# Optimization experiments

Hardware: AMD Instinct MI355X
Metric: run time of the kernel (lower is better)

Reference implementation:

```python
import jax, jax.numpy as jnp
import numpy as np

B, T_ENC, D_IN = 64, 32, 4096
T_DEC, D_WORD = 20, 300
H = 512
VOCAB = 20000


def lstm_scan(x_tbd, W, b, c0, h0):
    """TF BasicLSTMCell (forget_bias=1.0, gate order i,j,f,o) scanned over time.
    x_tbd: [T,B,D]; W: [D+H, 4H]; returns (c,h) final state and all h [T,B,H]."""
    def step(carry, x):
        c, h = carry
        z = jnp.concatenate([x, h], axis=-1) @ W + b  # [B,4H]
        i, j, f, o = jnp.split(z, 4, axis=-1)
        c = c * jax.nn.sigmoid(f + 1.0) + jax.nn.sigmoid(i) * jnp.tanh(j)
        h = jnp.tanh(c) * jax.nn.sigmoid(o)
        return (c, h), h
    (c, h), hs = jax.lax.scan(step, (c0, h0), x_tbd)
    return (c, h), hs


def setup_inputs() -> dict:
    key = jax.random.key(0)
    ks = jax.random.split(key, 8)
    frames = jax.random.normal(ks[0], (B, T_ENC, D_IN), dtype=jnp.float32)
    caption = jax.random.randint(ks[1], (B, T_DEC), 0, VOCAB, dtype=jnp.int32)
    embeddings = jax.random.normal(ks[2], (VOCAB, D_WORD), dtype=jnp.float32) * 0.1
    s_enc = 1.0 / np.sqrt(D_IN + H)
    s_dec = 1.0 / np.sqrt(D_WORD + H)
    W_enc = jax.random.normal(ks[3], (D_IN + H, 4 * H), dtype=jnp.float32) * s_enc
    b_enc = jnp.zeros((4 * H,), dtype=jnp.float32)
    W_dec = jax.random.normal(ks[4], (D_WORD + H, 4 * H), dtype=jnp.float32) * s_dec
    b_dec = jnp.zeros((4 * H,), dtype=jnp.float32)
    W_proj = jax.random.normal(ks[5], (H, D_WORD), dtype=jnp.float32) / np.sqrt(H)
    b_proj = jnp.zeros((D_WORD,), dtype=jnp.float32)
    return {"frames": frames, "embeddings": embeddings, "W_enc": W_enc,
            "b_enc": b_enc, "W_dec": W_dec, "b_dec": b_dec,
            "W_proj": W_proj, "b_proj": b_proj, "caption": caption}


def reference(frames, embeddings, W_enc, b_enc, W_dec, b_dec, W_proj, b_proj, caption):
    b = frames.shape[0]
    c0 = jnp.zeros((b, H), dtype=frames.dtype)
    h0 = jnp.zeros((b, H), dtype=frames.dtype)
    # encoder over frames (dropout keep_prob=1 -> identity)
    (c, h), _ = lstm_scan(jnp.swapaxes(frames, 0, 1), W_enc, b_enc, c0, h0)
    # teacher-forced decoder over caption embeddings
    cap_emb = embeddings[caption]                      # [B,T_dec,D_word]
    _, hs = lstm_scan(jnp.swapaxes(cap_emb, 0, 1), W_dec, b_dec, c, h)  # [T,B,H]
    # per-step shared dense hidden->word, vectorized over time
    word_vecs = hs @ W_proj + b_proj                   # [T,B,D_word]
    return jnp.swapaxes(word_vecs, 0, 1)               # [B,T_dec,D_word]
```

## Files before the change

kernel.cpp:

```cpp
#include <hip/hip_runtime.h>
#include <hip/hip_bf16.h>

#define BATCH  64
#define T_ENC  32
#define D_IN   4096
#define T_DEC  20
#define D_WORD 300
#define HID    512
#define FOURH  2048
#define NWG    64
#define FPAD   32
#define ZP     13
#define CNT_BASE 2048
#define FLAGS_N  3520

typedef __attribute__((ext_vector_type(8))) short short8;
typedef __attribute__((ext_vector_type(4))) float f32x4;
typedef unsigned long long ull;

static __device__ __forceinline__ unsigned short f2bf(float f){
  union { float f; unsigned u; } v; v.f = f;
  unsigned r = v.u + 0x7fffu + ((v.u >> 16) & 1u);
  return (unsigned short)(r >> 16);
}
static __device__ __forceinline__ float bf2f(unsigned short b){
  union { unsigned u; float f; } v; v.u = ((unsigned)b) << 16;
  return v.f;
}
static __device__ __forceinline__ float sigm(float x){
  return __builtin_amdgcn_rcpf(1.f + __expf(-x));
}
static __device__ __forceinline__ float tanh_f(float x){
  float e = __expf(2.f * x);
  return 1.f - 2.f * __builtin_amdgcn_rcpf(e + 1.f);
}

__global__ __launch_bounds__(256) void prep(
    const float* __restrict__ frames, const float* __restrict__ W_enc,
    unsigned short* __restrict__ fb, unsigned short* __restrict__ wt,
    unsigned* __restrict__ flags, float* __restrict__ Xe)
{
  const int g = blockIdx.x * 256 + threadIdx.x;
  if (blockIdx.x == 0){
    for (int i = threadIdx.x; i < FLAGS_N; i += 256)
      __hip_atomic_store(&flags[i], 0u, __ATOMIC_RELAXED, __HIP_MEMORY_SCOPE_AGENT);
  }
  {
    float2 z2; z2.x = 0.f; z2.y = 0.f;
    *(float2*)(Xe + (long)g * 2) = z2;
  }
  if (g < 1048576){
    const long base = (long)g * 8;
    float4 x0 = *(const float4*)(frames + base);
    float4 x1 = *(const float4*)(frames + base + 4);
    short8 v;
    v[0] = (short)f2bf(x0.x); v[1] = (short)f2bf(x0.y);
    v[2] = (short)f2bf(x0.z); v[3] = (short)f2bf(x0.w);
    v[4] = (short)f2bf(x1.x); v[5] = (short)f2bf(x1.y);
    v[6] = (short)f2bf(x1.z); v[7] = (short)f2bf(x1.w);
    *(short8*)(fb + base) = v;
  } else {
    const int r  = g - 1048576;
    const int k0 = (r >> 11) << 3;
    const int c  = r & 2047;
    short8 v;
#pragma unroll
    for (int j = 0; j < 8; ++j)
      v[j] = (short)f2bf(W_enc[(long)(k0 + j) * FOURH + c]);
    *(short8*)&wt[(long)c * D_IN + k0] = v;
  }
}

__device__ __forceinline__ void enc_tile8(
    int bx, int by, int kc,
    const unsigned short* __restrict__ A0, const unsigned short* __restrict__ Wt,
    float* Z, char* smem, unsigned* flags)
{
  char* As = smem;
  char* Bs = smem + 16384;
  const int tid = threadIdx.x;
  const int row0 = bx * 128, col0 = by * 128;

  const int ar = tid >> 2, ah = tid & 3;
  long asrc;
  {
    int R = row0 + ar;
    int b = R & 63, t = R >> 6;
    asrc = (long)(b * T_ENC + t) * D_IN;
  }
  const int bc = tid & 127, bh = tid >> 7;
  const long bsrc = (long)(col0 + bc) * D_IN;
  const long kbase = (long)kc * 1024;

  const int wave = tid >> 6, lane = tid & 63;
  const int wm = (wave >> 2) * 64, wn = (wave & 3) * 32;
  const int lr = lane & 15, lkb = (lane >> 4) << 4, lq = (lane >> 4) << 2;

  f32x4 acc[4][2];
#pragma unroll
  for (int m = 0; m < 4; ++m)
#pragma unroll
    for (int n = 0; n < 2; ++n) acc[m][n] = (f32x4){0.f, 0.f, 0.f, 0.f};

#define ELOAD8(DA, DB, IT) do { \
    const long ka = kbase + (long)(IT) * 64 + ah * 16; \
    const long kb = kbase + (long)(IT) * 64 + bh * 16; \
    _Pragma("unroll") \
    for (int j = 0; j < 2; ++j){ \
      DA[j] = *(const short8*)(A0 + asrc + ka + j * 8); \
      DB[j] = *(const short8*)(Wt + bsrc + kb + j * 8); \
    } \
  } while (0)

  short8 aR[2], bR[2];
  ELOAD8(aR, bR, 0);

  for (int it = 0; it < 16; ++it){
    __syncthreads();
#pragma unroll
    for (int j = 0; j < 2; ++j){
      *(short8*)(As + ar * 128 + ((ah * 32 + j * 16) ^ ((ar & 7) << 4))) = aR[j];
      *(short8*)(Bs + bc * 128 + ((bh * 32 + j * 16) ^ ((bc & 7) << 4))) = bR[j];
    }
    __syncthreads();
    short8 aN[2], bN[2];
    if (it < 15) ELOAD8(aN, bN, it + 1);
#pragma unroll
    for (int kk = 0; kk < 2; ++kk){
      short8 af[4], bfv[2];
#pragma unroll
      for (int m = 0; m < 4; ++m){
        const int r = wm + m * 16 + lr;
        af[m] = *(const short8*)(As + r * 128 + ((kk * 64 + lkb) ^ ((r & 7) << 4)));
      }
#pragma unroll
      for (int n = 0; n < 2; ++n){
        const int r = wn + n * 16 + lr;
        bfv[n] = *(const short8*)(Bs + r * 128 + ((kk * 64 + lkb) ^ ((r & 7) << 4)));
      }
#pragma unroll
      for (int m = 0; m < 4; ++m)
#pragma unroll
        for (int n = 0; n < 2; ++n)
          acc[m][n] = __builtin_amdgcn_mfma_f32_16x16x32_bf16(af[m], bfv[n], acc[m][n], 0, 0, 0);
    }
    if (it < 15){
      aR[0] = aN[0]; aR[1] = aN[1]; bR[0] = bN[0]; bR[1] = bN[1];
    }
  }
#undef ELOAD8

#pragma unroll
  for (int m = 0; m < 4; ++m)
#pragma unroll
    for (int n = 0; n < 2; ++n)
#pragma unroll
      for (int r = 0; r < 4; ++r){
        int gr = row0 + wm + m * 16 + lq + r;
        int gc = col0 + wn + n * 16 + lr;
        __hip_atomic_fetch_add(&Z[(long)gr * FOURH + gc], acc[m][n][r],
                               __ATOMIC_RELAXED, __HIP_MEMORY_SCOPE_AGENT);
      }
  __syncthreads();
  if (tid == 0)
    __hip_atomic_fetch_add(&flags[CNT_BASE + bx * 32], 1u,
                           __ATOMIC_RELAXED, __HIP_MEMORY_SCOPE_AGENT);
}

__device__ __forceinline__ void dec_tile8(
    int bx, int by, const float* __restrict__ emb, const int* __restrict__ cap,
    const float* __restrict__ W, float* Z, char* smem, unsigned* flags)
{
  constexpr int KLIM  = D_WORD;
  constexpr int ITERS = (KLIM + 31) / 32;
  short* As = (short*)smem;
  short* Bs = (short*)(smem + 10240);
  const int tid = threadIdx.x;
  const int row0 = bx * 128, col0 = by * 128;

  const int ar = tid >> 2, akq = (tid & 3) * 8;
  long asrc;
  {
    int R = row0 + ar;
    int b = R & 63, t = R >> 6;
    asrc = (long)cap[b * T_DEC + t] * D_WORD;
  }
  const int bc = tid & 127, bkq = (tid >> 7) * 8;

  const int wave = tid >> 6, lane = tid & 63;
  const int wm = (wave >> 2) * 64, wn = (wave & 3) * 32;
  const int lr = lane & 15, lk = (lane >> 4) << 3, lq = (lane >> 4) << 2;

  f32x4 acc[4][2];
#pragma unroll
  for (int m = 0; m < 4; ++m)
#pragma unroll
    for (int n = 0; n < 2; ++n) acc[m][n] = (f32x4){0.f, 0.f, 0.f, 0.f};

  for (int it = 0; it < ITERS; ++it){
    const int k0 = it * 32;
    float av[8], bv[8];
#pragma unroll
    for (int i = 0; i < 8; ++i){
      int k = k0 + akq + i;
      av[i] = (k < KLIM) ? emb[asrc + k] : 0.f;
    }
#pragma unroll
    for (int i = 0; i < 8; ++i){
      int k = k0 + bkq + i;
      bv[i] = (k < KLIM) ? W[(long)k * FOURH + col0 + bc] : 0.f;
    }
    __syncthreads();
    short8 a8, b8;
#pragma unroll
    for (int i = 0; i < 8; ++i){
      a8[i] = (short)f2bf(av[i]);  b8[i] = (short)f2bf(bv[i]);
    }
    *(short8*)&As[ar * 40 + akq] = a8;
    *(short8*)&Bs[bc * 40 + bkq] = b8;
    __syncthreads();
    short8 af[4], bfv[2];
#pragma unroll
    for (int m = 0; m < 4; ++m) af[m]  = *(const short8*)&As[(wm + m * 16 + lr) * 40 + lk];
#pragma unroll
    for (int n = 0; n < 2; ++n) bfv[n] = *(const short8*)&Bs[(wn + n * 16 + lr) * 40 + lk];
#pragma unroll
    for (int m = 0; m < 4; ++m)
#pragma unroll
      for (int n = 0; n < 2; ++n)
        acc[m][n] = __builtin_amdgcn_mfma_f32_16x16x32_bf16(af[m], bfv[n], acc[m][n], 0, 0, 0);
  }

#pragma unroll
  for (int m = 0; m < 4; ++m)
#pragma unroll
    for (int n = 0; n < 2; ++n)
#pragma unroll
      for (int r = 0; r < 4; ++r){
        int gr = row0 + wm + m * 16 + lq + r;
        int gc = col0 + wn + n * 16 + lr;
        __hip_atomic_store(&Z[(long)gr * FOURH + gc], acc[m][n][r],
                           __ATOMIC_RELAXED, __HIP_MEMORY_SCOPE_AGENT);
      }
  __syncthreads();
  if (tid == 0)
    __hip_atomic_fetch_add(&flags[CNT_BASE + (16 + bx) * 32], 1u,
                           __ATOMIC_RELAXED, __HIP_MEMORY_SCOPE_AGENT);
}

__device__ __forceinline__ void proj_tail(
    int p, const unsigned short* __restrict__ hsd, const float* __restrict__ Wp,
    const float* __restrict__ bp, float* __restrict__ out,
    unsigned* flags, char* smem)
{
  float* hl = (float*)smem;
  const int tid = threadIdx.x;
  const int r0 = p * 16;
  const int t  = r0 >> 6;

  {
    unsigned* dc = &flags[CNT_BASE + (26 + t) * 32];
    while (__hip_atomic_load(dc, __ATOMIC_RELAXED, __HIP_MEMORY_SCOPE_AGENT) < 64u)
      __builtin_amdgcn_s_sleep(16);
  }
  __builtin_amdgcn_sched_barrier(0);

  for (int idx = tid; idx < 16 * 512; idx += 512)
    hl[idx] = bf2f(hsd[(long)r0 * 512 + idx]);
  __syncthreads();
  if (tid < D_WORD){
    const int d = tid;
    float acc[16];
#pragma unroll
    for (int r = 0; r < 16; ++r) acc[r] = bp[d];
    for (int k = 0; k < 512; ++k){
      float w = Wp[k * D_WORD + d];
#pragma unroll
      for (int r = 0; r < 16; ++r) acc[r] += hl[r * 512 + k] * w;
    }
#pragma unroll
    for (int r = 0; r < 16; ++r){
      int R = r0 + r;
      int tt = R >> 6, b = R & 63;
      out[(long)(b * T_DEC + tt) * D_WORD + d] = acc[r];
    }
  }
}

#define REC_GEMM(WREG) do { \
  _Pragma("unroll") \
  for (int kk = 0; kk < 8; ++kk){ \
    short8 af; \
    ((ull*)&af)[0] = ha[2 * kk]; \
    ((ull*)&af)[1] = ha[2 * kk + 1]; \
    _Pragma("unroll") \
    for (int n = 0; n < 2; ++n) \
      acc[n] = __builtin_amdgcn_mfma_f32_16x16x32_bf16(af, WREG[kk][n], acc[n], 0, 0, 0); \
  } \
} while (0)

__global__ __launch_bounds__(512, 1) void fused(
    const unsigned short* __restrict__ fbf, const unsigned short* __restrict__ wbf,
    float* Xe,
    const float* __restrict__ emb, const int* __restrict__ cap,
    const float* __restrict__ W_dec, float* Xd,
    const float* __restrict__ Wre, const float* __restrict__ Wrd,
    const float* __restrict__ b_enc, const float* __restrict__ b_dec,
    const float* __restrict__ Wp, const float* __restrict__ bp,
    float* __restrict__ out,
    unsigned* hbuf_u, unsigned* hsd_u, unsigned* flags)
{
  __shared__ __align__(16) char smem[65536];
  const int bid = blockIdx.x;

  if (bid >= 64){
    int g = bid - 64;
    if (g < 512)        enc_tile8(g >> 6, g & 15, (g >> 4) & 3, fbf, wbf, Xe, smem, flags);
    else if (g < 672){  int d = g - 512; dec_tile8(d >> 4, d & 15, emb, cap, W_dec, Xd, smem, flags); }
    else if (g < 1184){ int e = g - 672; enc_tile8(8 + (e >> 6), e & 15, (e >> 4) & 3, fbf, wbf, Xe, smem, flags); }
    else                proj_tail(g - 1184, (const unsigned short*)hsd_u, Wp, bp, out, flags, smem);
    return;
  }

  float* zlds = (float*)smem;
  const int tid = threadIdx.x, wgid = bid;
  const int wave = tid >> 6, lane = tid & 63;
  const int kh = wave >> 2, mh = wave & 3;
  const int lr = lane & 15, lk = (lane >> 4) << 3;
  const int hi = lane >> 4, lq = (lane >> 4) << 2;

  int ocol[2];
#pragma unroll
  for (int n = 0; n < 2; ++n)
    ocol[n] = (n * 2 + (lr >> 3)) * 512 + wgid * 8 + (lr & 7);

  short8 we[8][2], wd[8][2];
#pragma unroll
  for (int kk = 0; kk < 8; ++kk)
#pragma unroll
    for (int n = 0; n < 2; ++n){
      short8 e, d;
#pragma unroll
      for (int j = 0; j < 8; ++j){
        int k = kh * 256 + kk * 32 + lk + j;
        e[j] = (short)f2bf(Wre[(long)k * FOURH + ocol[n]]);
        d[j] = (short)f2bf(Wrd[(long)k * FOURH + ocol[n]]);
      }
      we[kk][n] = e; wd[kk][n] = d;
    }

  const int cb_ = tid >> 3, cu = tid & 7;
  float c_reg = 0.f;

  float be4[4], bd4[4];
#pragma unroll
  for (int gg = 0; gg < 4; ++gg){
    be4[gg] = b_enc[gg * 512 + wgid * 8 + cu];
    bd4[gg] = b_dec[gg * 512 + wgid * 8 + cu];
  }

  if (tid < 128)
    __hip_atomic_store((ull*)hbuf_u + wgid * 128 + tid, 0ull,
                       __ATOMIC_RELAXED, __HIP_MEMORY_SCOPE_AGENT);
  __syncthreads();
  if (tid == 0)
    __hip_atomic_store(&flags[wgid * FPAD], 1u,
                       __ATOMIC_RELAXED, __HIP_MEMORY_SCOPE_AGENT);

  const bool mine = (lane != wgid);
  const int b2 = (mh * 16 + lr) * 2;

  for (int q = 0; q < T_ENC + T_DEC; ++q){
    const bool dec = (q >= T_ENC);
    const int tt = dec ? q - T_ENC : q;
    float* Xp = dec ? Xd : Xe;

    if (!(tt & 1)){
      unsigned* xc = dec ? &flags[CNT_BASE + (16 + (tt >> 1)) * 32]
                         : &flags[CNT_BASE + (tt >> 1) * 32];
      const unsigned xtgt = dec ? 16u : 64u;
      while (__hip_atomic_load(xc, __ATOMIC_RELAXED, __HIP_MEMORY_SCOPE_AGENT) < xtgt)
        __builtin_amdgcn_s_sleep(2);
    }
    __builtin_amdgcn_sched_barrier(0);

    const long xb = (long)(tt * BATCH + cb_) * FOURH + wgid * 8 + cu;
    float xi = __hip_atomic_load(&Xp[xb],        __ATOMIC_RELAXED, __HIP_MEMORY_SCOPE_AGENT);
    float xj = __hip_atomic_load(&Xp[xb +  512], __ATOMIC_RELAXED, __HIP_MEMORY_SCOPE_AGENT);
    float xf = __hip_atomic_load(&Xp[xb + 1024], __ATOMIC_RELAXED, __HIP_MEMORY_SCOPE_AGENT);
    float xo = __hip_atomic_load(&Xp[xb + 1536], __ATOMIC_RELAXED, __HIP_MEMORY_SCOPE_AGENT);

    {
      const unsigned tgt = (unsigned)(q + 1);
      for (;;){
        unsigned f = tgt;
        if (mine) f = __hip_atomic_load(&flags[lane * FPAD],
                                        __ATOMIC_RELAXED, __HIP_MEMORY_SCOPE_AGENT);
        if (__all((int)(f >= tgt))) break;
        __builtin_amdgcn_s_sleep(1);
      }
    }
    __builtin_amdgcn_sched_barrier(0);

    const ull* rb = (const ull*)hbuf_u + (q & 1) * 8192;
    ull ha[16];
#pragma unroll
    for (int kk = 0; kk < 8; ++kk){
      const int o = (kh * 32 + kk * 4 + hi) * 128 + b2;
      ha[2 * kk]     = __hip_atomic_load(rb + o,     __ATOMIC_RELAXED, __HIP_MEMORY_SCOPE_AGENT);
      ha[2 * kk + 1] = __hip_atomic_load(rb + o + 1, __ATOMIC_RELAXED, __HIP_MEMORY_SCOPE_AGENT);
    }

    f32x4 acc[2];
#pragma unroll
    for (int n = 0; n < 2; ++n) acc[n] = (f32x4){0.f, 0.f, 0.f, 0.f};
    __builtin_amdgcn_s_setprio(1);
    if (!dec) REC_GEMM(we); else REC_GEMM(wd);
    __builtin_amdgcn_s_setprio(0);

#pragma unroll
    for (int n = 0; n < 2; ++n){
      const int g = n * 2 + (lr >> 3), u = lr & 7;
#pragma unroll
      for (int r = 0; r < 4; ++r){
        const int row = mh * 16 + lq + r;
        zlds[((kh * 4 + g) * 64 + row) * ZP + u] = acc[n][r];
      }
    }
    __syncthreads();

    const int zb = cb_ * ZP + cu;
    float zi = zlds[(0 * 64) * ZP + zb] + zlds[(4 * 64) * ZP + zb] + xi + (dec ? bd4[0] : be4[0]);
    float zj = zlds[(1 * 64) * ZP + zb] + zlds[(5 * 64) * ZP + zb] + xj + (dec ? bd4[1] : be4[1]);
    float zf = zlds[(2 * 64) * ZP + zb] + zlds[(6 * 64) * ZP + zb] + xf + (dec ? bd4[2] : be4[2]);
    float zo = zlds[(3 * 64) * ZP + zb] + zlds[(7 * 64) * ZP + zb] + xo + (dec ? bd4[3] : be4[3]);
    c_reg = c_reg * sigm(zf + 1.f) + sigm(zi) * tanh_f(zj);
    float hn = tanh_f(c_reg) * sigm(zo);
    unsigned short hb = f2bf(hn);

    __hip_atomic_store(&((unsigned short*)hbuf_u)[((q + 1) & 1) * 32768 + wgid * 512 + tid],
                       hb, __ATOMIC_RELAXED, __HIP_MEMORY_SCOPE_AGENT);
    if (dec)
      __hip_atomic_store(&((unsigned short*)hsd_u)[(tt * BATCH + cb_) * 512 + wgid * 8 + cu],
                         hb, __ATOMIC_RELAXED, __HIP_MEMORY_SCOPE_AGENT);

    __syncthreads();
    if (tid == 0)
      __hip_atomic_store(&flags[wgid * FPAD], (unsigned)(q + 2),
                         __ATOMIC_RELAXED, __HIP_MEMORY_SCOPE_AGENT);
    if (dec && tid == 64)
      __hip_atomic_fetch_add(&flags[CNT_BASE + (26 + tt) * 32], 1u,
                             __ATOMIC_RELAXED, __HIP_MEMORY_SCOPE_AGENT);
  }
}

extern "C" void kernel_launch(void* const* d_in, const int* in_sizes, int n_in,
                              void* d_out, int out_size, void* d_ws, size_t ws_size,
                              hipStream_t stream)
{
  const float* frames  = (const float*)d_in[0];
  const float* emb     = (const float*)d_in[1];
  const float* W_enc   = (const float*)d_in[2];
  const float* b_enc   = (const float*)d_in[3];
  const float* W_dec   = (const float*)d_in[4];
  const float* b_dec   = (const float*)d_in[5];
  const float* W_proj  = (const float*)d_in[6];
  const float* b_proj  = (const float*)d_in[7];
  const int*   caption = (const int*)d_in[8];

  char* ws = (char*)d_ws;
  float*          Xe    = (float*)(ws + 0);
  float*          Xd    = (float*)(ws + 16777216);
  unsigned*       hbuf  = (unsigned*)(ws + 27262976);
  unsigned*       hsd   = (unsigned*)(ws + 27394048);
  unsigned*       flags = (unsigned*)(ws + 28704768);
  unsigned short* fbf   = (unsigned short*)(ws + 28721152);
  unsigned short* wbf   = (unsigned short*)(ws + 45498368);
  float* out = (float*)d_out;

  prep<<<8192, 256, 0, stream>>>(frames, W_enc, fbf, wbf, flags, Xe);
  fused<<<64 + 1184 + 80, 512, 0, stream>>>(
      fbf, wbf, Xe, emb, caption, W_dec, Xd,
      W_enc + (long)D_IN * FOURH,
      W_dec + (long)D_WORD * FOURH,
      b_enc, b_dec, W_proj, b_proj, out,
      hbuf, hsd, flags);
}
```

Before: 295.1 us.

## Replace per-step flag barriers with tagged hidden-state words for dataflow sync

Each hidden-state bf16 value is now stored in a 32-bit word with the step index in the upper half, so consumers poll the data itself instead of per-workgroup flags and counters. This removes the flag store, the extra syncthreads before it, and the separate hidden-state load after the wait, which should shorten the critical path of each recurrent step. Decoder recurrent weights are loaded into the same registers at the encoder/decoder switch to free registers, and the projection tail also polls tagged data. The cost is twice the hidden-buffer traffic and wider polling loads on every step.

```diff
diff --git a/kernel.cpp b/kernel.cpp
--- a/kernel.cpp
+++ b/kernel.cpp
@@ -9,7 +9,6 @@
 #define HID    512
 #define FOURH  2048
 #define NWG    64
-#define FPAD   32
 #define ZP     13
 #define CNT_BASE 2048
 #define FLAGS_N  3520
@@ -17,6 +16,8 @@
 typedef __attribute__((ext_vector_type(8))) short short8;
 typedef __attribute__((ext_vector_type(4))) float f32x4;
 typedef unsigned long long ull;
+
+#define TAGMASK 0xFFFF0000FFFF0000ull
 
 static __device__ __forceinline__ unsigned short f2bf(float f){
   union { float f; unsigned u; } v; v.f = f;
@@ -34,17 +35,25 @@
   float e = __expf(2.f * x);
   return 1.f - 2.f * __builtin_amdgcn_rcpf(e + 1.f);
 }
+static __device__ __forceinline__ unsigned pk2(ull h){
+  return (unsigned)(h & 0xFFFFu) | ((unsigned)(h >> 32) << 16);
+}
 
 __global__ __launch_bounds__(256) void prep(
     const float* __restrict__ frames, const float* __restrict__ W_enc,
     unsigned short* __restrict__ fb, unsigned short* __restrict__ wt,
-    unsigned* __restrict__ flags, float* __restrict__ Xe)
+    unsigned* __restrict__ flags, float* __restrict__ Xe,
+    unsigned* __restrict__ hbuf, unsigned* __restrict__ hsd)
 {
   const int g = blockIdx.x * 256 + threadIdx.x;
   if (blockIdx.x == 0){
     for (int i = threadIdx.x; i < FLAGS_N; i += 256)
       __hip_atomic_store(&flags[i], 0u, __ATOMIC_RELAXED, __HIP_MEMORY_SCOPE_AGENT);
   }
+  if (g < 65536)
+    __hip_atomic_store(&hbuf[g], 0u, __ATOMIC_RELAXED, __HIP_MEMORY_SCOPE_AGENT);
+  if (g < 655360)
+    __hip_atomic_store(&hsd[g], 0u, __ATOMIC_RELAXED, __HIP_MEMORY_SCOPE_AGENT);
   {
     float2 z2; z2.x = 0.f; z2.y = 0.f;
     *(float2*)(Xe + (long)g * 2) = z2;
@@ -249,24 +258,34 @@
 }
 
 __device__ __forceinline__ void proj_tail(
-    int p, const unsigned short* __restrict__ hsd, const float* __restrict__ Wp,
-    const float* __restrict__ bp, float* __restrict__ out,
-    unsigned* flags, char* smem)
+    int p, const unsigned* __restrict__ hsd, const float* __restrict__ Wp,
+    const float* __restrict__ bp, float* __restrict__ out, char* smem)
 {
   float* hl = (float*)smem;
   const int tid = threadIdx.x;
   const int r0 = p * 16;
   const int t  = r0 >> 6;
 
-  {
-    unsigned* dc = &flags[CNT_BASE + (26 + t) * 32];
-    while (__hip_atomic_load(dc, __ATOMIC_RELAXED, __HIP_MEMORY_SCOPE_AGENT) < 64u)
-      __builtin_amdgcn_s_sleep(16);
+  const ull* hp = (const ull*)hsd + (long)r0 * 256 + tid * 8;
+  const ull pat = ((ull)(unsigned)(t + 1) << 16) | ((ull)(unsigned)(t + 1) << 48);
+  ull v[8];
+  for (;;){
+    int ok = 1;
+#pragma unroll
+    for (int j = 0; j < 8; ++j)
+      v[j] = __hip_atomic_load(hp + j, __ATOMIC_RELAXED, __HIP_MEMORY_SCOPE_AGENT);
+#pragma unroll
+    for (int j = 0; j < 8; ++j)
+      ok &= (int)(((v[j] ^ pat) & TAGMASK) == 0);
+    if (__all(ok)) break;
+    __builtin_amdgcn_s_sleep(8);
   }
   __builtin_amdgcn_sched_barrier(0);
-
-  for (int idx = tid; idx < 16 * 512; idx += 512)
-    hl[idx] = bf2f(hsd[(long)r0 * 512 + idx]);
+#pragma unroll
+  for (int j = 0; j < 8; ++j){
+    hl[tid * 16 + 2 * j]     = bf2f((unsigned short)(v[j] & 0xFFFFu));
+    hl[tid * 16 + 2 * j + 1] = bf2f((unsigned short)((v[j] >> 32) & 0xFFFFu));
+  }
   __syncthreads();
   if (tid < D_WORD){
     const int d = tid;
@@ -290,12 +309,11 @@
 #define REC_GEMM(WREG) do { \
   _Pragma("unroll") \
   for (int kk = 0; kk < 8; ++kk){ \
-    short8 af; \
-    ((ull*)&af)[0] = ha[2 * kk]; \
-    ((ull*)&af)[1] = ha[2 * kk + 1]; \
+    union { unsigned u[4]; short8 s8; } uf; \
+    uf.u[0] = pka[kk]; uf.u[1] = pkb[kk]; uf.u[2] = pkc[kk]; uf.u[3] = pkd[kk]; \
     _Pragma("unroll") \
     for (int n = 0; n < 2; ++n) \
-      acc[n] = __builtin_amdgcn_mfma_f32_16x16x32_bf16(af, WREG[kk][n], acc[n], 0, 0, 0); \
+      acc[n] = __builtin_amdgcn_mfma_f32_16x16x32_bf16(uf.s8, WREG[kk][n], acc[n], 0, 0, 0); \
   } \
 } while (0)
 
@@ -310,7 +328,7 @@
     float* __restrict__ out,
     unsigned* hbuf_u, unsigned* hsd_u, unsigned* flags)
 {
-  __shared__ __align__(16) char smem[65536];
+  __shared__ __align__(16) char smem[32768];
   const int bid = blockIdx.x;
 
   if (bid >= 64){
@@ -318,7 +336,7 @@
     if (g < 512)        enc_tile8(g >> 6, g & 15, (g >> 4) & 3, fbf, wbf, Xe, smem, flags);
     else if (g < 672){  int d = g - 512; dec_tile8(d >> 4, d & 15, emb, cap, W_dec, Xd, smem, flags); }
     else if (g < 1184){ int e = g - 672; enc_tile8(8 + (e >> 6), e & 15, (e >> 4) & 3, fbf, wbf, Xe, smem, flags); }
-    else                proj_tail(g - 1184, (const unsigned short*)hsd_u, Wp, bp, out, flags, smem);
+    else                proj_tail(g - 1184, hsd_u, Wp, bp, out, smem);
     return;
   }
 
@@ -334,19 +352,18 @@
   for (int n = 0; n < 2; ++n)
     ocol[n] = (n * 2 + (lr >> 3)) * 512 + wgid * 8 + (lr & 7);
 
-  short8 we[8][2], wd[8][2];
+  short8 we[8][2];
 #pragma unroll
   for (int kk = 0; kk < 8; ++kk)
 #pragma unroll
     for (int n = 0; n < 2; ++n){
-      short8 e, d;
+      short8 e;
 #pragma unroll
       for (int j = 0; j < 8; ++j){
         int k = kh * 256 + kk * 32 + lk + j;
         e[j] = (short)f2bf(Wre[(long)k * FOURH + ocol[n]]);
-        d[j] = (short)f2bf(Wrd[(long)k * FOURH + ocol[n]]);
-      }
-      we[kk][n] = e; wd[kk][n] = d;
+      }
+      we[kk][n] = e;
     }
 
   const int cb_ = tid >> 3, cu = tid & 7;
@@ -359,21 +376,30 @@
     bd4[gg] = b_dec[gg * 512 + wgid * 8 + cu];
   }
 
-  if (tid < 128)
-    __hip_atomic_store((ull*)hbuf_u + wgid * 128 + tid, 0ull,
-                       __ATOMIC_RELAXED, __HIP_MEMORY_SCOPE_AGENT);
-  __syncthreads();
-  if (tid == 0)
-    __hip_atomic_store(&flags[wgid * FPAD], 1u,
-                       __ATOMIC_RELAXED, __HIP_MEMORY_SCOPE_AGENT);
-
-  const bool mine = (lane != wgid);
-  const int b2 = (mh * 16 + lr) * 2;
+  int off8[8];
+#pragma unroll
+  for (int kk = 0; kk < 8; ++kk)
+    off8[kk] = (kh * 32 + kk * 4 + hi) * 256 + (mh * 16 + lr) * 4;
 
   for (int q = 0; q < T_ENC + T_DEC; ++q){
     const bool dec = (q >= T_ENC);
     const int tt = dec ? q - T_ENC : q;
     float* Xp = dec ? Xd : Xe;
+
+    if (q == T_ENC){
+#pragma unroll
+      for (int kk = 0; kk < 8; ++kk)
+#pragma unroll
+        for (int n = 0; n < 2; ++n){
+          short8 d;
+#pragma unroll
+          for (int j = 0; j < 8; ++j){
+            int k = kh * 256 + kk * 32 + lk + j;
+            d[j] = (short)f2bf(Wrd[(long)k * FOURH + ocol[n]]);
+          }
+          we[kk][n] = d;
+        }
+    }
 
     if (!(tt & 1)){
       unsigned* xc = dec ? &flags[CNT_BASE + (16 + (tt >> 1)) * 32]
@@ -390,33 +416,59 @@
     float xf = __hip_atomic_load(&Xp[xb + 1024], __ATOMIC_RELAXED, __HIP_MEMORY_SCOPE_AGENT);
     float xo = __hip_atomic_load(&Xp[xb + 1536], __ATOMIC_RELAXED, __HIP_MEMORY_SCOPE_AGENT);
 
+    const ull* rb = (const ull*)hbuf_u + (q & 1) * 16384;
+    const ull pat = ((ull)(unsigned)q << 16) | ((ull)(unsigned)q << 48);
+    unsigned pka[8], pkb[8], pkc[8], pkd[8];
     {
-      const unsigned tgt = (unsigned)(q + 1);
+      ull h0[8];
       for (;;){
-        unsigned f = tgt;
-        if (mine) f = __hip_atomic_load(&flags[lane * FPAD],
-                                        __ATOMIC_RELAXED, __HIP_MEMORY_SCOPE_AGENT);
-        if (__all((int)(f >= tgt))) break;
+        int ok = 1;
+#pragma unroll
+        for (int kk = 0; kk < 8; ++kk)
+          h0[kk] = __hip_atomic_load(rb + off8[kk], __ATOMIC_RELAXED, __HIP_MEMORY_SCOPE_AGENT);
+#pragma unroll
+        for (int kk = 0; kk < 8; ++kk)
+          ok &= (int)(((h0[kk] ^ pat) & TAGMASK) == 0);
+        if (__all(ok)) break;
         __builtin_amdgcn_s_sleep(1);
       }
+#pragma unroll
+      for (int kk = 0; kk < 8; ++kk) pka[kk] = pk2(h0[kk]);
+    }
+    for (;;){
+      ull t1[8], t2[8], t3[8];
+      int ok = 1;
+#pragma unroll
+      for (int kk = 0; kk < 8; ++kk){
+        t1[kk] = __hip_atomic_load(rb + off8[kk] + 1, __ATOMIC_RELAXED, __HIP_MEMORY_SCOPE_AGENT);
+        t2[kk] = __hip_atomic_load(rb + off8[kk] + 2, __ATOMIC_RELAXED, __HIP_MEMORY_SCOPE_AGENT);
+        t3[kk] = __hip_atomic_load(rb + off8[kk] + 3, __ATOMIC_RELAXED, __HIP_MEMORY_SCOPE_AGENT);
+      }
+#pragma unroll
+      for (int kk = 0; kk < 8; ++kk){
+        ok &= (int)(((t1[kk] ^ pat) & TAGMASK) == 0);
+        ok &= (int)(((t2[kk] ^ pat) & TAGMASK) == 0);
+        ok &= (int)(((t3[kk] ^ pat) & TAGMASK) == 0);
+      }
+      if (__all(ok)){
+#pragma unroll
+        for (int kk = 0; kk < 8; ++kk){
+          pkb[kk] = pk2(t1[kk]); pkc[kk] = pk2(t2[kk]); pkd[kk] = pk2(t3[kk]);
+        }
+        break;
+      }
+      __builtin_amdgcn_s_sleep(1);
     }
     __builtin_amdgcn_sched_barrier(0);
-
-    const ull* rb = (const ull*)hbuf_u + (q & 1) * 8192;
-    ull ha[16];
-#pragma unroll
-    for (int kk = 0; kk < 8; ++kk){
-      const int o = (kh * 32 + kk * 4 + hi) * 128 + b2;
-      ha[2 * kk]     = __hip_atomic_load(rb + o,     __ATOMIC_RELAXED, __HIP_MEMORY_SCOPE_AGENT);
-      ha[2 * kk + 1] = __hip_atomic_load(rb + o + 1, __ATOMIC_RELAXED, __HIP_MEMORY_SCOPE_AGENT);
-    }
 
     f32x4 acc[2];
 #pragma unroll
     for (int n = 0; n < 2; ++n) acc[n] = (f32x4){0.f, 0.f, 0.f, 0.f};
     __builtin_amdgcn_s_setprio(1);
-    if (!dec) REC_GEMM(we); else REC_GEMM(wd);
+    REC_GEMM(we);
     __builtin_amdgcn_s_setprio(0);
+
+    __syncthreads();
 
 #pragma unroll
     for (int n = 0; n < 2; ++n){
@@ -438,19 +490,13 @@
     float hn = tanh_f(c_reg) * sigm(zo);
     unsigned short hb = f2bf(hn);
 
-    __hip_atomic_store(&((unsigned short*)hbuf_u)[((q + 1) & 1) * 32768 + wgid * 512 + tid],
-                       hb, __ATOMIC_RELAXED, __HIP_MEMORY_SCOPE_AGENT);
+    __hip_atomic_store(&hbuf_u[((q + 1) & 1) * 32768 + wgid * 512 + tid],
+                       ((unsigned)(q + 1) << 16) | (unsigned)hb,
+                       __ATOMIC_RELAXED, __HIP_MEMORY_SCOPE_AGENT);
     if (dec)
-      __hip_atomic_store(&((unsigned short*)hsd_u)[(tt * BATCH + cb_) * 512 + wgid * 8 + cu],
-                         hb, __ATOMIC_RELAXED, __HIP_MEMORY_SCOPE_AGENT);
-
-    __syncthreads();
-    if (tid == 0)
-      __hip_atomic_store(&flags[wgid * FPAD], (unsigned)(q + 2),
+      __hip_atomic_store(&hsd_u[(long)(tt * BATCH + cb_) * 512 + wgid * 8 + cu],
+                         ((unsigned)(tt + 1) << 16) | (unsigned)hb,
                          __ATOMIC_RELAXED, __HIP_MEMORY_SCOPE_AGENT);
-    if (dec && tid == 64)
-      __hip_atomic_fetch_add(&flags[CNT_BASE + (26 + tt) * 32], 1u,
-                             __ATOMIC_RELAXED, __HIP_MEMORY_SCOPE_AGENT);
   }
 }
 
@@ -472,13 +518,13 @@
   float*          Xe    = (float*)(ws + 0);
   float*          Xd    = (float*)(ws + 16777216);
   unsigned*       hbuf  = (unsigned*)(ws + 27262976);
-  unsigned*       hsd   = (unsigned*)(ws + 27394048);
-  unsigned*       flags = (unsigned*)(ws + 28704768);
-  unsigned short* fbf   = (unsigned short*)(ws + 28721152);
-  unsigned short* wbf   = (unsigned short*)(ws + 45498368);
+  unsigned*       hsd   = (unsigned*)(ws + 27525120);
+  unsigned*       flags = (unsigned*)(ws + 30146560);
+  unsigned short* fbf   = (unsigned short*)(ws + 30162944);
+  unsigned short* wbf   = (unsigned short*)(ws + 46940160);
   float* out = (float*)d_out;
 
-  prep<<<8192, 256, 0, stream>>>(frames, W_enc, fbf, wbf, flags, Xe);
+  prep<<<8192, 256, 0, stream>>>(frames, W_enc, fbf, wbf, flags, Xe, hbuf, hsd);
   fused<<<64 + 1184 + 80, 512, 0, stream>>>(
       fbf, wbf, Xe, emb, caption, W_dec, Xd,
       W_enc + (long)D_IN * FOURH,
```

New measurement: 407.7 us. 1.38x slower.

## Restructure recurrent LSTM step to per-wave gates with per-wave flags, no LDS

Applied to the files above, without the earlier changes.

Each wave now computes a full 16x16 tile over the whole K=512 and holds all four gates for its units, so the gate assembly uses cross-lane shuffles instead of an LDS round trip and a __syncthreads. Completion is published per wave through 512 separate flags, so consumers poll two flags per lane and no workgroup barrier is needed. The decoder recurrent weights are loaded into the same registers when the encoder finishes, which lowers register pressure and allows launch bounds of 4 blocks per CU with a smaller LDS array. In exchange there is more flag polling traffic, a stall at the encoder-to-decoder switch while the weights reload, and the flag and workspace layout has to move to make room.

```diff
diff --git a/kernel.cpp b/kernel.cpp
--- a/kernel.cpp
+++ b/kernel.cpp
@@ -9,10 +9,9 @@
 #define HID    512
 #define FOURH  2048
 #define NWG    64
-#define FPAD   32
 #define ZP     13
-#define CNT_BASE 2048
-#define FLAGS_N  3520
+#define CNT_BASE 16384
+#define FLAGS_N  17856
 
 typedef __attribute__((ext_vector_type(8))) short short8;
 typedef __attribute__((ext_vector_type(4))) float f32x4;
@@ -260,7 +259,7 @@
 
   {
     unsigned* dc = &flags[CNT_BASE + (26 + t) * 32];
-    while (__hip_atomic_load(dc, __ATOMIC_RELAXED, __HIP_MEMORY_SCOPE_AGENT) < 64u)
+    while (__hip_atomic_load(dc, __ATOMIC_RELAXED, __HIP_MEMORY_SCOPE_AGENT) < 512u)
       __builtin_amdgcn_s_sleep(16);
   }
   __builtin_amdgcn_sched_barrier(0);
@@ -287,19 +286,7 @@
   }
 }
 
-#define REC_GEMM(WREG) do { \
-  _Pragma("unroll") \
-  for (int kk = 0; kk < 8; ++kk){ \
-    short8 af; \
-    ((ull*)&af)[0] = ha[2 * kk]; \
-    ((ull*)&af)[1] = ha[2 * kk + 1]; \
-    _Pragma("unroll") \
-    for (int n = 0; n < 2; ++n) \
-      acc[n] = __builtin_amdgcn_mfma_f32_16x16x32_bf16(af, WREG[kk][n], acc[n], 0, 0, 0); \
-  } \
-} while (0)
-
-__global__ __launch_bounds__(512, 1) void fused(
+__global__ __launch_bounds__(512, 4) void fused(
     const unsigned short* __restrict__ fbf, const unsigned short* __restrict__ wbf,
     float* Xe,
     const float* __restrict__ emb, const int* __restrict__ cap,
@@ -310,7 +297,7 @@
     float* __restrict__ out,
     unsigned* hbuf_u, unsigned* hsd_u, unsigned* flags)
 {
-  __shared__ __align__(16) char smem[65536];
+  __shared__ __align__(16) char smem[32768];
   const int bid = blockIdx.x;
 
   if (bid >= 64){
@@ -322,58 +309,57 @@
     return;
   }
 
-  float* zlds = (float*)smem;
   const int tid = threadIdx.x, wgid = bid;
-  const int wave = tid >> 6, lane = tid & 63;
-  const int kh = wave >> 2, mh = wave & 3;
-  const int lr = lane & 15, lk = (lane >> 4) << 3;
-  const int hi = lane >> 4, lq = (lane >> 4) << 2;
-
-  int ocol[2];
-#pragma unroll
-  for (int n = 0; n < 2; ++n)
-    ocol[n] = (n * 2 + (lr >> 3)) * 512 + wgid * 8 + (lr & 7);
-
-  short8 we[8][2], wd[8][2];
-#pragma unroll
-  for (int kk = 0; kk < 8; ++kk)
-#pragma unroll
-    for (int n = 0; n < 2; ++n){
-      short8 e, d;
-#pragma unroll
-      for (int j = 0; j < 8; ++j){
-        int k = kh * 256 + kk * 32 + lk + j;
-        e[j] = (short)f2bf(Wre[(long)k * FOURH + ocol[n]]);
-        d[j] = (short)f2bf(Wrd[(long)k * FOURH + ocol[n]]);
-      }
-      we[kk][n] = e; wd[kk][n] = d;
-    }
-
-  const int cb_ = tid >> 3, cu = tid & 7;
-  float c_reg = 0.f;
-
-  float be4[4], bd4[4];
-#pragma unroll
-  for (int gg = 0; gg < 4; ++gg){
-    be4[gg] = b_enc[gg * 512 + wgid * 8 + cu];
-    bd4[gg] = b_dec[gg * 512 + wgid * 8 + cu];
-  }
-
-  if (tid < 128)
-    __hip_atomic_store((ull*)hbuf_u + wgid * 128 + tid, 0ull,
+  const int w = tid >> 6, lane = tid & 63;
+  const int bg = w & 3, uh = w >> 2;
+  const int c = lane & 15, hi4 = lane >> 4;
+  const int g = c >> 2;
+  const int u = uh * 4 + (c & 3);
+  const int col4h = g * 512 + wgid * 8 + u;
+  unsigned short* hb16 = (unsigned short*)hbuf_u;
+  unsigned short* hs16 = (unsigned short*)hsd_u;
+
+  short8 wv[16];
+#pragma unroll
+  for (int ks = 0; ks < 16; ++ks){
+    short8 e;
+#pragma unroll
+    for (int j = 0; j < 8; ++j)
+      e[j] = (short)f2bf(Wre[(long)(ks * 32 + hi4 * 8 + j) * FOURH + col4h]);
+    wv[ks] = e;
+  }
+  const float be1 = b_enc[col4h], bd1 = b_dec[col4h];
+  float c_reg[4] = {0.f, 0.f, 0.f, 0.f};
+
+  const bool pub = (c < 4);
+  if (pub){
+#pragma unroll
+    for (int r = 0; r < 4; ++r)
+      __hip_atomic_store(&hb16[wgid * 512 + (bg * 16 + hi4 * 4 + r) * 8 + uh * 4 + c],
+                         (unsigned short)0, __ATOMIC_RELAXED, __HIP_MEMORY_SCOPE_AGENT);
+  }
+  asm volatile("s_waitcnt vmcnt(0)" ::: "memory");
+  if (lane == 0)
+    __hip_atomic_store(&flags[(wgid * 8 + w) * 32], 1u,
                        __ATOMIC_RELAXED, __HIP_MEMORY_SCOPE_AGENT);
-  __syncthreads();
-  if (tid == 0)
-    __hip_atomic_store(&flags[wgid * FPAD], 1u,
-                       __ATOMIC_RELAXED, __HIP_MEMORY_SCOPE_AGENT);
-
-  const bool mine = (lane != wgid);
-  const int b2 = (mh * 16 + lr) * 2;
+
+  const int obase = hi4 * 128 + (bg * 16 + c) * 2;
 
   for (int q = 0; q < T_ENC + T_DEC; ++q){
     const bool dec = (q >= T_ENC);
     const int tt = dec ? q - T_ENC : q;
-    float* Xp = dec ? Xd : Xe;
+    const float* Xp = dec ? Xd : Xe;
+
+    if (q == T_ENC){
+#pragma unroll
+      for (int ks = 0; ks < 16; ++ks){
+        short8 d;
+#pragma unroll
+        for (int j = 0; j < 8; ++j)
+          d[j] = (short)f2bf(Wrd[(long)(ks * 32 + hi4 * 8 + j) * FOURH + col4h]);
+        wv[ks] = d;
+      }
+    }
 
     if (!(tt & 1)){
       unsigned* xc = dec ? &flags[CNT_BASE + (16 + (tt >> 1)) * 32]
@@ -384,71 +370,73 @@
     }
     __builtin_amdgcn_sched_barrier(0);
 
-    const long xb = (long)(tt * BATCH + cb_) * FOURH + wgid * 8 + cu;
-    float xi = __hip_atomic_load(&Xp[xb],        __ATOMIC_RELAXED, __HIP_MEMORY_SCOPE_AGENT);
-    float xj = __hip_atomic_load(&Xp[xb +  512], __ATOMIC_RELAXED, __HIP_MEMORY_SCOPE_AGENT);
-    float xf = __hip_atomic_load(&Xp[xb + 1024], __ATOMIC_RELAXED, __HIP_MEMORY_SCOPE_AGENT);
-    float xo = __hip_atomic_load(&Xp[xb + 1536], __ATOMIC_RELAXED, __HIP_MEMORY_SCOPE_AGENT);
+    float xg[4];
+#pragma unroll
+    for (int r = 0; r < 4; ++r)
+      xg[r] = __hip_atomic_load(
+          &Xp[(long)(tt * BATCH + bg * 16 + hi4 * 4 + r) * FOURH + col4h],
+          __ATOMIC_RELAXED, __HIP_MEMORY_SCOPE_AGENT);
 
     {
       const unsigned tgt = (unsigned)(q + 1);
       for (;;){
-        unsigned f = tgt;
-        if (mine) f = __hip_atomic_load(&flags[lane * FPAD],
+        unsigned f0 = __hip_atomic_load(&flags[(lane * 8 + bg) * 32],
                                         __ATOMIC_RELAXED, __HIP_MEMORY_SCOPE_AGENT);
-        if (__all((int)(f >= tgt))) break;
+        unsigned f1 = __hip_atomic_load(&flags[(lane * 8 + bg + 4) * 32],
+                                        __ATOMIC_RELAXED, __HIP_MEMORY_SCOPE_AGENT);
+        if (__all((int)(f0 >= tgt && f1 >= tgt))) break;
         __builtin_amdgcn_s_sleep(1);
       }
     }
     __builtin_amdgcn_sched_barrier(0);
 
     const ull* rb = (const ull*)hbuf_u + (q & 1) * 8192;
-    ull ha[16];
-#pragma unroll
-    for (int kk = 0; kk < 8; ++kk){
-      const int o = (kh * 32 + kk * 4 + hi) * 128 + b2;
-      ha[2 * kk]     = __hip_atomic_load(rb + o,     __ATOMIC_RELAXED, __HIP_MEMORY_SCOPE_AGENT);
-      ha[2 * kk + 1] = __hip_atomic_load(rb + o + 1, __ATOMIC_RELAXED, __HIP_MEMORY_SCOPE_AGENT);
-    }
-
-    f32x4 acc[2];
-#pragma unroll
-    for (int n = 0; n < 2; ++n) acc[n] = (f32x4){0.f, 0.f, 0.f, 0.f};
+    f32x4 acc = (f32x4){0.f, 0.f, 0.f, 0.f};
     __builtin_amdgcn_s_setprio(1);
-    if (!dec) REC_GEMM(we); else REC_GEMM(wd);
+#pragma unroll
+    for (int ks = 0; ks < 16; ++ks){
+      const int o = ks * 512 + obase;
+      ull h0 = __hip_atomic_load(rb + o,     __ATOMIC_RELAXED, __HIP_MEMORY_SCOPE_AGENT);
+      ull h1 = __hip_atomic_load(rb + o + 1, __ATOMIC_RELAXED, __HIP_MEMORY_SCOPE_AGENT);
+      union { ull q2[2]; short8 s; } uf; uf.q2[0] = h0; uf.q2[1] = h1;
+      acc = __builtin_amdgcn_mfma_f32_16x16x32_bf16(uf.s, wv[ks], acc, 0, 0, 0);
+    }
     __builtin_amdgcn_s_setprio(0);
 
-#pragma unroll
-    for (int n = 0; n < 2; ++n){
-      const int g = n * 2 + (lr >> 3), u = lr & 7;
+    unsigned short hbv[4];
+#pragma unroll
+    for (int r = 0; r < 4; ++r){
+      float v = acc[r] + xg[r] + (dec ? bd1 : be1);
+      float s4 = __shfl_xor(v, 4);
+      float lo  = (g & 1) ? s4 : v;
+      float hi_ = (g & 1) ? v  : s4;
+      float lo8 = __shfl_xor(lo, 8);
+      float hi8 = __shfl_xor(hi_, 8);
+      float vzi = (g & 2) ? lo8 : lo;
+      float vzf = (g & 2) ? lo  : lo8;
+      float vzj = (g & 2) ? hi8 : hi_;
+      float vzo = (g & 2) ? hi_ : hi8;
+      c_reg[r] = c_reg[r] * sigm(vzf + 1.f) + sigm(vzi) * tanh_f(vzj);
+      float hn = tanh_f(c_reg[r]) * sigm(vzo);
+      hbv[r] = f2bf(hn);
+    }
+
+    if (pub){
 #pragma unroll
       for (int r = 0; r < 4; ++r){
-        const int row = mh * 16 + lq + r;
-        zlds[((kh * 4 + g) * 64 + row) * ZP + u] = acc[n][r];
-      }
-    }
-    __syncthreads();
-
-    const int zb = cb_ * ZP + cu;
-    float zi = zlds[(0 * 64) * ZP + zb] + zlds[(4 * 64) * ZP + zb] + xi + (dec ? bd4[0] : be4[0]);
-    float zj = zlds[(1 * 64) * ZP + zb] + zlds[(5 * 64) * ZP + zb] + xj + (dec ? bd4[1] : be4[1]);
-    float zf = zlds[(2 * 64) * ZP + zb] + zlds[(6 * 64) * ZP + zb] + xf + (dec ? bd4[2] : be4[2]);
-    float zo = zlds[(3 * 64) * ZP + zb] + zlds[(7 * 64) * ZP + zb] + xo + (dec ? bd4[3] : be4[3]);
-    c_reg = c_reg * sigm(zf + 1.f) + sigm(zi) * tanh_f(zj);
-    float hn = tanh_f(c_reg) * sigm(zo);
-    unsigned short hb = f2bf(hn);
-
-    __hip_atomic_store(&((unsigned short*)hbuf_u)[((q + 1) & 1) * 32768 + wgid * 512 + tid],
-                       hb, __ATOMIC_RELAXED, __HIP_MEMORY_SCOPE_AGENT);
-    if (dec)
-      __hip_atomic_store(&((unsigned short*)hsd_u)[(tt * BATCH + cb_) * 512 + wgid * 8 + cu],
-                         hb, __ATOMIC_RELAXED, __HIP_MEMORY_SCOPE_AGENT);
-
-    __syncthreads();
-    if (tid == 0)
-      __hip_atomic_store(&flags[wgid * FPAD], (unsigned)(q + 2),
+        const int b = bg * 16 + hi4 * 4 + r;
+        __hip_atomic_store(&hb16[((q + 1) & 1) * 32768 + wgid * 512 + b * 8 + uh * 4 + c],
+                           hbv[r], __ATOMIC_RELAXED, __HIP_MEMORY_SCOPE_AGENT);
+        if (dec)
+          __hip_atomic_store(&hs16[(long)(tt * BATCH + b) * 512 + wgid * 8 + uh * 4 + c],
+                             hbv[r], __ATOMIC_RELAXED, __HIP_MEMORY_SCOPE_AGENT);
+      }
+    }
+    asm volatile("s_waitcnt vmcnt(0)" ::: "memory");
+    if (lane == 0)
+      __hip_atomic_store(&flags[(wgid * 8 + w) * 32], (unsigned)(q + 2),
                          __ATOMIC_RELAXED, __HIP_MEMORY_SCOPE_AGENT);
-    if (dec && tid == 64)
+    if (dec && lane == 1)
       __hip_atomic_fetch_add(&flags[CNT_BASE + (26 + tt) * 32], 1u,
                              __ATOMIC_RELAXED, __HIP_MEMORY_SCOPE_AGENT);
   }
@@ -474,8 +462,8 @@
   unsigned*       hbuf  = (unsigned*)(ws + 27262976);
   unsigned*       hsd   = (unsigned*)(ws + 27394048);
   unsigned*       flags = (unsigned*)(ws + 28704768);
-  unsigned short* fbf   = (unsigned short*)(ws + 28721152);
-  unsigned short* wbf   = (unsigned short*)(ws + 45498368);
+  unsigned short* fbf   = (unsigned short*)(ws + 28778496);
+  unsigned short* wbf   = (unsigned short*)(ws + 45555712);
   float* out = (float*)d_out;
 
   prep<<<8192, 256, 0, stream>>>(frames, W_enc, fbf, wbf, flags, Xe);
```

New measurement: 770.4 us. 2.61x slower.

## Partition recurrent LSTM by batch groups to shrink per-step flag dependencies

Applied to the files above, without the earlier changes.

Each of the 64 recurrent workgroups now owns 16 batch rows by 32 hidden units instead of all 64 batch rows by 8 hidden units. It therefore only needs h from the 16 workgroups in its batch group, and polls 16 flags instead of 63 each step. The point is to cut the global all-to-all barrier to a 16-way one and let batch groups run ahead independently. The hbuf layout changes to a batch-major order, the LDS reduction uses a new padded layout, and the static LDS drops to 32 KB.

```diff
diff --git a/kernel.cpp b/kernel.cpp
--- a/kernel.cpp
+++ b/kernel.cpp
@@ -10,7 +10,6 @@
 #define FOURH  2048
 #define NWG    64
 #define FPAD   32
-#define ZP     13
 #define CNT_BASE 2048
 #define FLAGS_N  3520
 
@@ -289,13 +288,13 @@
 
 #define REC_GEMM(WREG) do { \
   _Pragma("unroll") \
-  for (int kk = 0; kk < 8; ++kk){ \
+  for (int ks = 0; ks < 8; ++ks){ \
     short8 af; \
-    ((ull*)&af)[0] = ha[2 * kk]; \
-    ((ull*)&af)[1] = ha[2 * kk + 1]; \
+    ((ull*)&af)[0] = ha[2 * ks]; \
+    ((ull*)&af)[1] = ha[2 * ks + 1]; \
     _Pragma("unroll") \
     for (int n = 0; n < 2; ++n) \
-      acc[n] = __builtin_amdgcn_mfma_f32_16x16x32_bf16(af, WREG[kk][n], acc[n], 0, 0, 0); \
+      acc[n] = __builtin_amdgcn_mfma_f32_16x16x32_bf16(af, WREG[ks][n], acc[n], 0, 0, 0); \
   } \
 } while (0)
 
@@ -310,7 +309,7 @@
     float* __restrict__ out,
     unsigned* hbuf_u, unsigned* hsd_u, unsigned* flags)
 {
-  __shared__ __align__(16) char smem[65536];
+  __shared__ __align__(16) char smem[32768];
   const int bid = blockIdx.x;
 
   if (bid >= 64){
@@ -324,56 +323,58 @@
 
   float* zlds = (float*)smem;
   const int tid = threadIdx.x, wgid = bid;
-  const int wave = tid >> 6, lane = tid & 63;
-  const int kh = wave >> 2, mh = wave & 3;
-  const int lr = lane & 15, lk = (lane >> 4) << 3;
-  const int hi = lane >> 4, lq = (lane >> 4) << 2;
+  const int bg = wgid >> 4, cs = wgid & 15;
+  const int w = tid >> 6, lane = tid & 63;
+  const int kh = w >> 2, ch = w & 3;
+  const int lr = lane & 15, hi4 = lane >> 4, lq = hi4 * 4;
+  unsigned short* hb16 = (unsigned short*)hbuf_u;
+  unsigned short* hs16 = (unsigned short*)hsd_u;
 
   int ocol[2];
 #pragma unroll
   for (int n = 0; n < 2; ++n)
-    ocol[n] = (n * 2 + (lr >> 3)) * 512 + wgid * 8 + (lr & 7);
+    ocol[n] = ch * 512 + cs * 32 + n * 16 + lr;
 
   short8 we[8][2], wd[8][2];
 #pragma unroll
-  for (int kk = 0; kk < 8; ++kk)
+  for (int ks = 0; ks < 8; ++ks)
 #pragma unroll
     for (int n = 0; n < 2; ++n){
       short8 e, d;
 #pragma unroll
       for (int j = 0; j < 8; ++j){
-        int k = kh * 256 + kk * 32 + lk + j;
+        int k = kh * 256 + ks * 32 + hi4 * 8 + j;
         e[j] = (short)f2bf(Wre[(long)k * FOURH + ocol[n]]);
         d[j] = (short)f2bf(Wrd[(long)k * FOURH + ocol[n]]);
       }
-      we[kk][n] = e; wd[kk][n] = d;
-    }
-
-  const int cb_ = tid >> 3, cu = tid & 7;
+      we[ks][n] = e; wd[ks][n] = d;
+    }
+
+  const int b_ = tid >> 5, u_ = tid & 31;
   float c_reg = 0.f;
 
   float be4[4], bd4[4];
 #pragma unroll
   for (int gg = 0; gg < 4; ++gg){
-    be4[gg] = b_enc[gg * 512 + wgid * 8 + cu];
-    bd4[gg] = b_dec[gg * 512 + wgid * 8 + cu];
+    be4[gg] = b_enc[gg * 512 + cs * 32 + u_];
+    bd4[gg] = b_dec[gg * 512 + cs * 32 + u_];
   }
 
   if (tid < 128)
-    __hip_atomic_store((ull*)hbuf_u + wgid * 128 + tid, 0ull,
-                       __ATOMIC_RELAXED, __HIP_MEMORY_SCOPE_AGENT);
+    __hip_atomic_store((ull*)hbuf_u + (bg * 16 + (tid >> 3)) * 128 + cs * 8 + (tid & 7),
+                       0ull, __ATOMIC_RELAXED, __HIP_MEMORY_SCOPE_AGENT);
   __syncthreads();
   if (tid == 0)
     __hip_atomic_store(&flags[wgid * FPAD], 1u,
                        __ATOMIC_RELAXED, __HIP_MEMORY_SCOPE_AGENT);
 
-  const bool mine = (lane != wgid);
-  const int b2 = (mh * 16 + lr) * 2;
+  const int fsrc = (bg * 16 + (lane & 15)) * FPAD;
+  const int obase = (bg * 16 + lr) * 128 + kh * 64 + hi4 * 2;
 
   for (int q = 0; q < T_ENC + T_DEC; ++q){
     const bool dec = (q >= T_ENC);
     const int tt = dec ? q - T_ENC : q;
-    float* Xp = dec ? Xd : Xe;
+    const float* Xp = dec ? Xd : Xe;
 
     if (!(tt & 1)){
       unsigned* xc = dec ? &flags[CNT_BASE + (16 + (tt >> 1)) * 32]
@@ -384,7 +385,7 @@
     }
     __builtin_amdgcn_sched_barrier(0);
 
-    const long xb = (long)(tt * BATCH + cb_) * FOURH + wgid * 8 + cu;
+    const long xb = (long)(tt * BATCH + bg * 16 + b_) * FOURH + cs * 32 + u_;
     float xi = __hip_atomic_load(&Xp[xb],        __ATOMIC_RELAXED, __HIP_MEMORY_SCOPE_AGENT);
     float xj = __hip_atomic_load(&Xp[xb +  512], __ATOMIC_RELAXED, __HIP_MEMORY_SCOPE_AGENT);
     float xf = __hip_atomic_load(&Xp[xb + 1024], __ATOMIC_RELAXED, __HIP_MEMORY_SCOPE_AGENT);
@@ -393,9 +394,8 @@
     {
       const unsigned tgt = (unsigned)(q + 1);
       for (;;){
-        unsigned f = tgt;
-        if (mine) f = __hip_atomic_load(&flags[lane * FPAD],
-                                        __ATOMIC_RELAXED, __HIP_MEMORY_SCOPE_AGENT);
+        unsigned f = __hip_atomic_load(&flags[fsrc],
+                                       __ATOMIC_RELAXED, __HIP_MEMORY_SCOPE_AGENT);
         if (__all((int)(f >= tgt))) break;
         __builtin_amdgcn_s_sleep(1);
       }
@@ -405,10 +405,10 @@
     const ull* rb = (const ull*)hbuf_u + (q & 1) * 8192;
     ull ha[16];
 #pragma unroll
-    for (int kk = 0; kk < 8; ++kk){
-      const int o = (kh * 32 + kk * 4 + hi) * 128 + b2;
-      ha[2 * kk]     = __hip_atomic_load(rb + o,     __ATOMIC_RELAXED, __HIP_MEMORY_SCOPE_AGENT);
-      ha[2 * kk + 1] = __hip_atomic_load(rb + o + 1, __ATOMIC_RELAXED, __HIP_MEMORY_SCOPE_AGENT);
+    for (int ks = 0; ks < 8; ++ks){
+      const int o = obase + ks * 8;
+      ha[2 * ks]     = __hip_atomic_load(rb + o,     __ATOMIC_RELAXED, __HIP_MEMORY_SCOPE_AGENT);
+      ha[2 * ks + 1] = __hip_atomic_load(rb + o + 1, __ATOMIC_RELAXED, __HIP_MEMORY_SCOPE_AGENT);
     }
 
     f32x4 acc[2];
@@ -419,29 +419,24 @@
     __builtin_amdgcn_s_setprio(0);
 
 #pragma unroll
-    for (int n = 0; n < 2; ++n){
-      const int g = n * 2 + (lr >> 3), u = lr & 7;
-#pragma unroll
-      for (int r = 0; r < 4; ++r){
-        const int row = mh * 16 + lq + r;
-        zlds[((kh * 4 + g) * 64 + row) * ZP + u] = acc[n][r];
-      }
-    }
-    __syncthreads();
-
-    const int zb = cb_ * ZP + cu;
-    float zi = zlds[(0 * 64) * ZP + zb] + zlds[(4 * 64) * ZP + zb] + xi + (dec ? bd4[0] : be4[0]);
-    float zj = zlds[(1 * 64) * ZP + zb] + zlds[(5 * 64) * ZP + zb] + xj + (dec ? bd4[1] : be4[1]);
-    float zf = zlds[(2 * 64) * ZP + zb] + zlds[(6 * 64) * ZP + zb] + xf + (dec ? bd4[2] : be4[2]);
-    float zo = zlds[(3 * 64) * ZP + zb] + zlds[(7 * 64) * ZP + zb] + xo + (dec ? bd4[3] : be4[3]);
+    for (int n = 0; n < 2; ++n)
+#pragma unroll
+      for (int r = 0; r < 4; ++r)
+        zlds[((kh * 4 + ch) * 32 + n * 16 + lr) * 17 + lq + r] = acc[n][r];
+    __syncthreads();
+
+    float zi = zlds[((0 * 4 + 0) * 32 + u_) * 17 + b_] + zlds[((1 * 4 + 0) * 32 + u_) * 17 + b_] + xi + (dec ? bd4[0] : be4[0]);
+    float zj = zlds[((0 * 4 + 1) * 32 + u_) * 17 + b_] + zlds[((1 * 4 + 1) * 32 + u_) * 17 + b_] + xj + (dec ? bd4[1] : be4[1]);
+    float zf = zlds[((0 * 4 + 2) * 32 + u_) * 17 + b_] + zlds[((1 * 4 + 2) * 32 + u_) * 17 + b_] + xf + (dec ? bd4[2] : be4[2]);
+    float zo = zlds[((0 * 4 + 3) * 32 + u_) * 17 + b_] + zlds[((1 * 4 + 3) * 32 + u_) * 17 + b_] + xo + (dec ? bd4[3] : be4[3]);
     c_reg = c_reg * sigm(zf + 1.f) + sigm(zi) * tanh_f(zj);
     float hn = tanh_f(c_reg) * sigm(zo);
     unsigned short hb = f2bf(hn);
 
-    __hip_atomic_store(&((unsigned short*)hbuf_u)[((q + 1) & 1) * 32768 + wgid * 512 + tid],
+    __hip_atomic_store(&hb16[((q + 1) & 1) * 32768 + (bg * 16 + b_) * 512 + cs * 32 + u_],
                        hb, __ATOMIC_RELAXED, __HIP_MEMORY_SCOPE_AGENT);
     if (dec)
-      __hip_atomic_store(&((unsigned short*)hsd_u)[(tt * BATCH + cb_) * 512 + wgid * 8 + cu],
+      __hip_atomic_store(&hs16[(long)(tt * BATCH + bg * 16 + b_) * 512 + cs * 32 + u_],
                          hb, __ATOMIC_RELAXED, __HIP_MEMORY_SCOPE_AGENT);
 
     __syncthreads();
```

New measurement: 366.8 us. 24.3% more time.
